# Optimization experiments

Hardware: AMD Instinct MI355X
Metric: run time of the kernel (lower is better)

Reference implementation:

```python
import jax, jax.numpy as jnp
import numpy as np

B, N, E_PER = 2048, 64, 512            # graphs, nodes/graph, edges/graph
D_NODE, D_EMB = 16, 64                 # env.node_state_dim, node_embedding_size
D_USER, D_UEMB = 32, 64                # env.user_state_dim, user_embedding_size
HID = 512
TOTAL_N, TOTAL_E = B * N, B * E_PER


def setup_inputs() -> dict:
    key = jax.random.key(0)
    ks = jax.random.split(key, 16)
    off = (jnp.arange(B, dtype=jnp.int32) * N)[:, None]
    src = jax.random.randint(ks[0], (B, E_PER), 0, N, dtype=jnp.int32) + off
    dst = jax.random.randint(ks[1], (B, E_PER), 0, N, dtype=jnp.int32) + off
    edge_index = jnp.stack([src.reshape(-1), dst.reshape(-1)])  # [2, TOTAL_E]
    s = lambda k, shape, sc=0.05: jax.random.normal(k, shape, jnp.float32) * sc
    return {
        "x": jax.random.normal(ks[2], (TOTAL_N, D_NODE), jnp.float32),
        "edge_attr": jax.random.normal(ks[3], (TOTAL_E, 2), jnp.float32),
        "user_s": jax.random.normal(ks[4], (B, D_USER), jnp.float32),
        "W_msg": s(ks[5], (D_NODE, D_EMB)), "b_msg": jnp.zeros((D_EMB,), jnp.float32),
        "W_edge": s(ks[6], (2, D_EMB)),     "b_edge": jnp.zeros((D_EMB,), jnp.float32),
        "W_self": s(ks[7], (D_NODE, D_EMB)),"b_self": jnp.zeros((D_EMB,), jnp.float32),
        "W1": s(ks[8], (D_USER, D_UEMB)),   "b1": jnp.zeros((D_UEMB,), jnp.float32),
        "W2": s(ks[9], (N * D_EMB + D_UEMB, HID)), "b2": jnp.zeros((HID,), jnp.float32),
        "W3": s(ks[10], (HID, HID // 2)),   "b3": jnp.zeros((HID // 2,), jnp.float32),
        "W4": s(ks[11], (HID // 2, N), 0.01), "b4": jnp.zeros((N,), jnp.float32),
        "edge_index": edge_index,
    }


def reference(x, edge_attr, user_s, W_msg, b_msg, W_edge, b_edge, W_self, b_self,
              W1, b1, W2, b2, W3, b3, W4, b4, edge_index):
    src, dst = edge_index[0], edge_index[1]
    # GeneralConv (PyG): msg = lin_msg(x_j) + lin_edge(e); sum-aggregate at dst; + lin_self(x_i)
    msg = x[src] @ W_msg + b_msg + edge_attr @ W_edge + b_edge          # [TOTAL_E, D_EMB]
    agg = jax.ops.segment_sum(msg, dst, num_segments=TOTAL_N)          # [TOTAL_N, D_EMB]
    node = jax.nn.relu(agg + x @ W_self + b_self)
    # F.dropout(p=0.5, training=True) -- deterministic mask for the reference
    keep = jax.random.bernoulli(jax.random.key(42), 0.5, node.shape)
    node = jnp.where(keep, node * 2.0, 0.0)
    user = jax.nn.relu(user_s @ W1 + b1)                               # [B, D_UEMB]
    states = jnp.concatenate([node.reshape(B, N * D_EMB), user], axis=1)
    h = jax.nn.relu(states @ W2 + b2)
    h = jax.nn.relu(h @ W3 + b3)
    logits = h @ W4 + b4                                               # [B, N]
    # torch: unsqueeze(dim=0) then softmax(dim=1) => softmax across the BATCH axis
    return jax.nn.softmax(logits, axis=0)[None]                        # [1, B, N]
```

## Files before the change

### kernel.cpp

```cpp
#include <hip/hip_runtime.h>
#include <stdint.h>

#define B_GRAPHS 2048
#define CHUNK 256
#define E_PER 512
#define D_USER 32
#define HID 512
#define GK 4160
#define STATES_DIM 4160
#define WS_FALLBACK 6356992
#define WS_FAST 52006912

typedef unsigned short u16;
typedef unsigned int u32;
typedef __attribute__((ext_vector_type(8))) short short8;
typedef __attribute__((ext_vector_type(4))) float f32x4;

__device__ __forceinline__ float bf2f(u16 b) {
    union { uint32_t u; float f; } c; c.u = ((uint32_t)b) << 16; return c.f;
}
__device__ __forceinline__ u16 f2bf(float f) {
    union { float f; uint32_t u; } c; c.f = f;
    uint32_t u = c.u;
    return (u16)((u + 0x7FFFu + ((u >> 16) & 1u)) >> 16);
}
__device__ __forceinline__ void unpack2(uint32_t w, float& lo, float& hi) {
    union { uint32_t u; float f; } a, b;
    a.u = w << 16; b.u = w & 0xFFFF0000u;
    lo = a.f; hi = b.f;
}

__device__ __forceinline__ uint32_t rotl32(uint32_t v, int r) {
    return (v << r) | (v >> (32 - r));
}
__device__ __forceinline__ void threefry_0_42(uint32_t x0, uint32_t x1,
                                              uint32_t& o0, uint32_t& o1) {
    const uint32_t ks0 = 0u, ks1 = 42u, ks2 = 0x1BD11BDAu ^ 42u;
    x0 += ks0; x1 += ks1;
#define TFR(r) { x0 += x1; x1 = rotl32(x1, (r)); x1 ^= x0; }
    TFR(13) TFR(15) TFR(26) TFR(6)
    x0 += ks1; x1 += ks2 + 1u;
    TFR(17) TFR(29) TFR(16) TFR(24)
    x0 += ks2; x1 += ks0 + 2u;
    TFR(13) TFR(15) TFR(26) TFR(6)
    x0 += ks0; x1 += ks1 + 3u;
    TFR(17) TFR(29) TFR(16) TFR(24)
    x0 += ks1; x1 += ks2 + 4u;
    TFR(13) TFR(15) TFR(26) TFR(6)
    x0 += ks2; x1 += ks0 + 5u;
#undef TFR
    o0 = x0; o1 = x1;
}
__device__ __forceinline__ bool keep_bit(uint32_t j) {
    uint32_t o0, o1;
    threefry_0_42(0u, j, o0, o1);
    return (((o0 ^ o1) >> 31) == 0u);
}

__global__ __launch_bounds__(256) void fill_kernel(float* __restrict__ out, float v, int n) {
    int i = blockIdx.x * 256 + threadIdx.x;
    if (i < n) out[i] = v;
}

__device__ __forceinline__ void trans32(float (*sT)[33],
                                        const float* __restrict__ W,
                                        u16* __restrict__ WT,
                                        int K, int N, int k0, int n0, int tid) {
    const int tr = tid >> 5, tc = tid & 31;
    #pragma unroll
    for (int i = 0; i < 32; i += 8)
        sT[tr + i][tc] = W[(size_t)(k0 + tr + i) * N + n0 + tc];
    __syncthreads();
    #pragma unroll
    for (int i = 0; i < 32; i += 8)
        WT[(size_t)(n0 + tr + i) * K + k0 + tc] = f2bf(sT[tc][tr + i]);
}

__global__ __launch_bounds__(256) void prep_kernel(
    const float* __restrict__ W2, u16* __restrict__ W2T,
    const float* __restrict__ W3, u16* __restrict__ W3T,
    const float* __restrict__ W4, u16* __restrict__ W4T,
    const float* __restrict__ W_msg, const float* __restrict__ W_self,
    u16* __restrict__ WcatT)
{
    __shared__ float sT[32][33];
    const int tid = threadIdx.x;
    int b = blockIdx.x;
    if (b < 2080) {
        trans32(sT, W2, W2T, 4160, 512, (b % 130) * 32, (b / 130) * 32, tid);
        return;
    }
    b -= 2080;
    if (b < 128) {
        trans32(sT, W3, W3T, 512, 256, (b % 16) * 32, (b / 16) * 32, tid);
        return;
    }
    b -= 128;
    if (b < 16) {
        trans32(sT, W4, W4T, 256, 64, (b % 8) * 32, (b / 8) * 32, tid);
        return;
    }
    #pragma unroll
    for (int i = 0; i < 8; ++i) {
        int idx = tid + 256 * i;
        int e = idx >> 5, k = idx & 31;
        float v = (k < 16) ? W_msg[k * 64 + e] : W_self[(k - 16) * 64 + e];
        WcatT[idx] = f2bf(v);
    }
}

__global__ __launch_bounds__(256) void node_fast(
    const float* __restrict__ x, const float* __restrict__ edge_attr,
    const float* __restrict__ user_s,
    const float* __restrict__ b_msg, const float* __restrict__ W_edge,
    const float* __restrict__ b_edge, const float* __restrict__ b_self,
    const float* __restrict__ W1, const float* __restrict__ b1,
    const int* __restrict__ src, const int* __restrict__ dst,
    const u16* __restrict__ WcatT,
    u16* __restrict__ states)
{
    const int g = blockIdx.x;
    const int tid = threadIdx.x;
    const int w = tid >> 6, lane = tid & 63;
    const int lm = lane & 15, q = lane >> 4;

    __shared__ u32 scnt[64][32];
    __shared__ u16 sxT[16][72];
    __shared__ u16 sA2[64][40];
    __shared__ float sesum[2][64];
    __shared__ float sdeg[64];
    __shared__ unsigned long long smask[64];

    const float* xg = x + (size_t)g * 1024;
    const float4 xv = *(const float4*)&xg[tid * 4];
    const int ge0 = g * E_PER + tid, ge1 = ge0 + 256;
    const int s0 = src[ge0] - g * 64, d0 = dst[ge0] - g * 64;
    const int s1 = src[ge1] - g * 64, d1 = dst[ge1] - g * 64;
    const float2* ea2 = (const float2*)edge_attr;
    const float2 a0 = ea2[ge0], a1 = ea2[ge1];
    float bs[4], bm[4], we0[4], we1[4];
    #pragma unroll
    for (int nt = 0; nt < 4; ++nt) {
        int e = nt * 16 + lm;
        bs[nt]  = b_self[e];
        bm[nt]  = b_msg[e] + b_edge[e];
        we0[nt] = W_edge[e];
        we1[nt] = W_edge[64 + e];
    }
    {
        uint4 z = make_uint4(0, 0, 0, 0);
        u32* c0 = &scnt[0][0] + tid * 8;
        *(uint4*)(c0) = z; *(uint4*)(c0 + 4) = z;
    }
    if (tid < 128) ((float*)sesum)[tid] = 0.f;
    {
        const int n = tid >> 2, kb = (tid & 3) * 4;
        u16 x0 = f2bf(xv.x), x1 = f2bf(xv.y), x2 = f2bf(xv.z), x3 = f2bf(xv.w);
        sxT[kb + 0][n] = x0; sxT[kb + 1][n] = x1;
        sxT[kb + 2][n] = x2; sxT[kb + 3][n] = x3;
        *(ushort4*)&sA2[n][16 + kb] = make_ushort4(x0, x1, x2, x3);
    }
    #pragma unroll 4
    for (int i = 0; i < 16; ++i) {
        unsigned long long b =
            __ballot(keep_bit((uint32_t)g * 4096u + (uint32_t)(i * 256 + tid)));
        if (lane == 0) smask[i * 4 + w] = b;
    }
    __syncthreads();

    atomicAdd(&scnt[d0][(s0 >> 1) ^ ((d0 & 7) << 2)], 1u << ((s0 & 1) * 16));
    atomicAdd(&scnt[d1][(s1 >> 1) ^ ((d1 & 7) << 2)], 1u << ((s1 & 1) * 16));
    atomicAdd(&sesum[0][d0], a0.x);
    atomicAdd(&sesum[1][d0], a0.y);
    atomicAdd(&sesum[0][d1], a1.x);
    atomicAdd(&sesum[1][d1], a1.y);
    __syncthreads();

    {
        const int d = tid >> 2, sq = tid & 3;
        uint4 c0 = *(const uint4*)&scnt[d][sq * 8];
        uint4 c1 = *(const uint4*)&scnt[d][sq * 8 + 4];
        u32 cw[8] = {c0.x, c0.y, c0.z, c0.w, c1.x, c1.y, c1.z, c1.w};
        u32 pk[8];
        float degp = 0.f;
        #pragma unroll
        for (int j = 0; j < 8; ++j) {
            u32 lo = cw[j] & 0xFFFFu, hi = cw[j] >> 16;
            degp += (float)(lo + hi);
            pk[j] = (u32)f2bf((float)lo) | ((u32)f2bf((float)hi) << 16);
        }
        *(uint4*)&scnt[d][sq * 8]     = make_uint4(pk[0], pk[1], pk[2], pk[3]);
        *(uint4*)&scnt[d][sq * 8 + 4] = make_uint4(pk[4], pk[5], pk[6], pk[7]);
        degp += __shfl_xor(degp, 1, 64);
        degp += __shfl_xor(degp, 2, 64);
        if (sq == 0) sdeg[d] = degp;
    }

    f32x4 accS;
    #pragma unroll
    for (int r = 0; r < 4; ++r) accS[r] = 0.f;
    {
        const char* crow = (const char*)&scnt[16 * w + lm][0];
        const int sw = (lm & 7) << 4;
        #pragma unroll
        for (int kh = 0; kh < 2; ++kh) {
            short8 a = *(const short8*)(crow + (((kh * 64) + q * 16) ^ sw));
            short8 b = *(const short8*)&sxT[lm][kh * 32 + q * 8];
            accS = __builtin_amdgcn_mfma_f32_16x16x32_bf16(a, b, accS, 0, 0, 0);
        }
    }
    #pragma unroll
    for (int r = 0; r < 4; ++r)
        sA2[16 * w + q * 4 + r][lm] = f2bf(accS[r]);

    f32x4 acc2[4];
    #pragma unroll
    for (int nt = 0; nt < 4; ++nt)
        #pragma unroll
        for (int r = 0; r < 4; ++r) acc2[nt][r] = 0.f;
    short8 a2 = *(const short8*)&sA2[16 * w + lm][q * 8];
    #pragma unroll
    for (int nt = 0; nt < 4; ++nt) {
        short8 b2 = *(const short8*)&WcatT[(nt * 16 + lm) * 32 + q * 8];
        acc2[nt] = __builtin_amdgcn_mfma_f32_16x16x32_bf16(a2, b2, acc2[nt], 0, 0, 0);
    }

    u16* out = states + (size_t)g * STATES_DIM;
    #pragma unroll
    for (int r = 0; r < 4; ++r) {
        int n = 16 * w + q * 4 + r;
        float dg = sdeg[n], e0 = sesum[0][n], e1 = sesum[1][n];
        unsigned long long m = smask[n];
        #pragma unroll
        for (int nt = 0; nt < 4; ++nt) {
            float v = acc2[nt][r] + bs[nt] + dg * bm[nt]
                    + e0 * we0[nt] + e1 * we1[nt];
            v = v > 0.f ? v : 0.f;
            int e = nt * 16 + lm;
            v = ((m >> e) & 1ull) ? v * 2.0f : 0.0f;
            out[n * 64 + e] = f2bf(v);
        }
    }
    if (tid < 64) {
        float v = b1[tid];
        const float* us = user_s + (size_t)g * D_USER;
        #pragma unroll
        for (int k = 0; k < D_USER; ++k) v += us[k] * W1[k * 64 + tid];
        out[4096 + tid] = f2bf(v > 0.f ? v : 0.f);
    }
}

__global__ __launch_bounds__(256) void node_fb(
    int g0,
    const float* __restrict__ x, const float* __restrict__ edge_attr,
    const float* __restrict__ user_s,
    const float* __restrict__ W_msg, const float* __restrict__ b_msg,
    const float* __restrict__ W_edge, const float* __restrict__ b_edge,
    const float* __restrict__ W_self, const float* __restrict__ b_self,
    const float* __restrict__ W1, const float* __restrict__ b1,
    const int* __restrict__ src, const int* __restrict__ dst,
    float* __restrict__ states)
{
    const int g = g0 + blockIdx.x;
    const int tid = threadIdx.x;

    __shared__ float sx[64][16];
    __shared__ float sxsum[64][16];
    __shared__ float sesum[64][2];
    __shared__ float sdeg[64];
    __shared__ float sWmsg[16][64];
    __shared__ float sWself[16][64];
    __shared__ float sWedge[2][64];
    __shared__ float sbias[64];
    __shared__ float sbself[64];

    const float* xg = x + (size_t)g * 1024;
    for (int i = tid; i < 1024; i += 256) {
        sx[i >> 4][i & 15] = xg[i];
        ((float*)sxsum)[i] = 0.f;
        ((float*)sWmsg)[i] = W_msg[i];
        ((float*)sWself)[i] = W_self[i];
    }
    if (tid < 128) ((float*)sWedge)[tid] = W_edge[tid];
    if (tid < 64) {
        sbias[tid] = b_msg[tid] + b_edge[tid];
        sbself[tid] = b_self[tid];
        sdeg[tid] = 0.f;
        sesum[tid][0] = 0.f; sesum[tid][1] = 0.f;
    }
    __syncthreads();

    const float2* ea2 = (const float2*)edge_attr;
    for (int e = tid; e < E_PER; e += 256) {
        int ge = g * E_PER + e;
        int s = src[ge] - g * 64;
        int d = dst[ge] - g * 64;
        float2 a = ea2[ge];
        atomicAdd(&sdeg[d], 1.0f);
        atomicAdd(&sesum[d][0], a.x);
        atomicAdd(&sesum[d][1], a.y);
        #pragma unroll
        for (int k = 0; k < 16; ++k) atomicAdd(&sxsum[d][k], sx[s][k]);
    }
    __syncthreads();

    float* out = states + (size_t)blockIdx.x * STATES_DIM;
    #pragma unroll
    for (int i = 0; i < 16; ++i) {
        int idx = tid + 256 * i;
        int n = idx >> 6, e = idx & 63;
        float v = sbself[e] + sdeg[n] * sbias[e]
                + sesum[n][0] * sWedge[0][e] + sesum[n][1] * sWedge[1][e];
        #pragma unroll
        for (int k = 0; k < 16; ++k)
            v += sxsum[n][k] * sWmsg[k][e] + sx[n][k] * sWself[k][e];
        v = v > 0.f ? v : 0.f;
        v = keep_bit((uint32_t)g * 4096u + (uint32_t)idx) ? v * 2.0f : 0.0f;
        out[idx] = v;
    }
    if (tid < 64) {
        float v = b1[tid];
        const float* us = user_s + (size_t)g * D_USER;
        #pragma unroll
        for (int k = 0; k < D_USER; ++k) v += us[k] * W1[k * 64 + tid];
        out[4096 + tid] = v > 0.f ? v : 0.f;
    }
}

__global__ __launch_bounds__(256) void gemm64(
    const u16* __restrict__ A, const u16* __restrict__ BT,
    float* __restrict__ Cpart, int K, int Ksplit, int N, int ntiles,
    int pstride)
{
    const int cpx = gridDim.x >> 3;
    const int bid = blockIdx.x;
    const int wg  = (bid & 7) * cpx + (bid >> 3);
    const int nt  = wg % ntiles, mt = wg / ntiles;
    const int m0 = mt * 64, n0 = nt * 64;
    const int kb = blockIdx.y * Ksplit;

    __shared__ u16 sA[64][72];
    __shared__ u16 sB[64][72];

    const int tid = threadIdx.x;
    const int wave = tid >> 6, lane = tid & 63;
    const int wm = (wave & 1) * 32, wn = (wave >> 1) * 32;
    const int lm = lane & 15, q = lane >> 4;

    f32x4 acc00, acc01, acc10, acc11;
    #pragma unroll
    for (int r = 0; r < 4; ++r) {
        acc00[r] = 0.f; acc01[r] = 0.f; acc10[r] = 0.f; acc11[r] = 0.f;
    }

    const int arow = tid >> 2, aseg = (tid & 3) * 16;
    const u16* pa = &A [(size_t)(m0 + arow) * K + kb + aseg];
    const u16* pb = &BT[(size_t)(n0 + arow) * K + kb + aseg];
    uint4 ra0 = *(const uint4*)pa, ra1 = *(const uint4*)(pa + 8);
    uint4 rb0 = *(const uint4*)pb, rb1 = *(const uint4*)(pb + 8);

    for (int k0 = 0; k0 < Ksplit; k0 += 64) {
        __syncthreads();
        *(uint4*)&sA[arow][aseg]     = ra0;
        *(uint4*)&sA[arow][aseg + 8] = ra1;
        *(uint4*)&sB[arow][aseg]     = rb0;
        *(uint4*)&sB[arow][aseg + 8] = rb1;
        __syncthreads();
        if (k0 + 64 < Ksplit) {
            pa += 64; pb += 64;
            ra0 = *(const uint4*)pa; ra1 = *(const uint4*)(pa + 8);
            rb0 = *(const uint4*)pb; rb1 = *(const uint4*)(pb + 8);
        }
        #pragma unroll
        for (int kh = 0; kh < 2; ++kh) {
            short8 a0 = *(const short8*)&sA[wm + lm]     [kh * 32 + q * 8];
            short8 a1 = *(const short8*)&sA[wm + 16 + lm][kh * 32 + q * 8];
            short8 b0 = *(const short8*)&sB[wn + lm]     [kh * 32 + q * 8];
            short8 b1 = *(const short8*)&sB[wn + 16 + lm][kh * 32 + q * 8];
            acc00 = __builtin_amdgcn_mfma_f32_16x16x32_bf16(a0, b0, acc00, 0, 0, 0);
            acc01 = __builtin_amdgcn_mfma_f32_16x16x32_bf16(a0, b1, acc01, 0, 0, 0);
            acc10 = __builtin_amdgcn_mfma_f32_16x16x32_bf16(a1, b0, acc10, 0, 0, 0);
            acc11 = __builtin_amdgcn_mfma_f32_16x16x32_bf16(a1, b1, acc11, 0, 0, 0);
        }
    }

    float* Cp = Cpart + (size_t)blockIdx.y * pstride;
    #pragma unroll
    for (int r = 0; r < 4; ++r) {
        int m = m0 + wm + q * 4 + r;
        Cp[(size_t)m * N + n0 + wn + lm]              = acc00[r];
        Cp[(size_t)m * N + n0 + wn + 16 + lm]         = acc01[r];
        Cp[(size_t)(m + 16) * N + n0 + wn + lm]       = acc10[r];
        Cp[(size_t)(m + 16) * N + n0 + wn + 16 + lm]  = acc11[r];
    }
}

__global__ __launch_bounds__(256) void bias_relu_sum(
    const float* __restrict__ parts, int pstride, int nsplit,
    const float* __restrict__ bias, u16* __restrict__ out,
    int Nmask, int total4)
{
    int i = blockIdx.x * 256 + threadIdx.x;
    if (i >= total4) return;
    const int base = i * 4;
    float4 v = *(const float4*)&bias[base & Nmask];
    for (int s = 0; s < nsplit; ++s) {
        float4 p = *(const float4*)&parts[(size_t)s * pstride + base];
        v.x += p.x; v.y += p.y; v.z += p.z; v.w += p.w;
    }
    ushort4 o;
    o.x = f2bf(v.x > 0.f ? v.x : 0.f);
    o.y = f2bf(v.y > 0.f ? v.y : 0.f);
    o.z = f2bf(v.z > 0.f ? v.z : 0.f);
    o.w = f2bf(v.w > 0.f ? v.w : 0.f);
    *(ushort4*)&out[base] = o;
}

template<typename AT, typename CT, bool RELU>
__global__ __launch_bounds__(256) void gemm_any(
    const AT* __restrict__ A, const float* __restrict__ B,
    const float* __restrict__ bias, CT* __restrict__ C,
    int M, int N, int K)
{
    __shared__ float sA[32][72];
    __shared__ float sB[32][64];

    const int tid = threadIdx.x;
    const int tx = tid & 15;
    const int ty = tid >> 4;
    const int m0 = blockIdx.x * 64, n0 = blockIdx.y * 64;

    float acc[4][4] = {};

    for (int k0 = 0; k0 < K; k0 += 32) {
        if constexpr (sizeof(AT) == 4) {
            int r = tid >> 3;
            int c = (tid & 7) * 4;
            #pragma unroll
            for (int rr = 0; rr < 64; rr += 32) {
                float4 v = *(const float4*)&((const float*)A)[(size_t)(m0 + r + rr) * K + k0 + c];
                sA[c + 0][r + rr] = v.x; sA[c + 1][r + rr] = v.y;
                sA[c + 2][r + rr] = v.z; sA[c + 3][r + rr] = v.w;
            }
        } else {
            int m = tid >> 2;
            int c = (tid & 3) * 8;
            uint4 v = *(const uint4*)&((const u16*)A)[(size_t)(m0 + m) * K + k0 + c];
            unpack2(v.x, sA[c + 0][m], sA[c + 1][m]);
            unpack2(v.y, sA[c + 2][m], sA[c + 3][m]);
            unpack2(v.z, sA[c + 4][m], sA[c + 5][m]);
            unpack2(v.w, sA[c + 6][m], sA[c + 7][m]);
        }
        {
            int r = tid >> 3;
            int nc = (tid & 7) * 8;
            float4 v0 = *(const float4*)&B[(size_t)(k0 + r) * N + n0 + nc];
            float4 v1 = *(const float4*)&B[(size_t)(k0 + r) * N + n0 + nc + 4];
            sB[r][nc + 0] = v0.x; sB[r][nc + 1] = v0.y;
            sB[r][nc + 2] = v0.z; sB[r][nc + 3] = v0.w;
            sB[r][nc + 4] = v1.x; sB[r][nc + 5] = v1.y;
            sB[r][nc + 6] = v1.z; sB[r][nc + 7] = v1.w;
        }
        __syncthreads();
        #pragma unroll
        for (int kk = 0; kk < 32; ++kk) {
            float4 av = *(const float4*)&sA[kk][ty * 4];
            float4 bv = *(const float4*)&sB[kk][tx * 4];
            float a_[4] = {av.x, av.y, av.z, av.w};
            float b_[4] = {bv.x, bv.y, bv.z, bv.w};
            #pragma unroll
            for (int i = 0; i < 4; ++i)
                #pragma unroll
                for (int j = 0; j < 4; ++j)
                    acc[i][j] += a_[i] * b_[j];
        }
        __syncthreads();
    }

    #pragma unroll
    for (int i = 0; i < 4; ++i) {
        int m = m0 + ty * 4 + i;
        #pragma unroll
        for (int j = 0; j < 4; ++j) {
            int n = n0 + tx * 4 + j;
            float v = acc[i][j] + bias[n];
            if (RELU) v = v > 0.f ? v : 0.f;
            if constexpr (sizeof(CT) == 2) C[(size_t)m * N + n] = (CT)f2bf(v);
            else                           C[(size_t)m * N + n] = (CT)v;
        }
    }
}

__global__ __launch_bounds__(256) void softmax4(
    const float* __restrict__ parts, const float* __restrict__ b4,
    float* __restrict__ out)
{
    const int n = blockIdx.x;
    const int tid = threadIdx.x;
    __shared__ float sred[4];
    const int wid = tid >> 6, lane = tid & 63;
    const float bn = b4[n];

    float v[8];
    #pragma unroll
    for (int i = 0; i < 8; ++i) {
        int row = (tid + 256 * i) * 64 + n;
        float t = bn + parts[row] + parts[131072 + row]
                + parts[262144 + row] + parts[393216 + row];
        v[i] = (t > -1e30f && t < 1e30f) ? t : 0.0f;
    }

    float mx = -3.4e38f;
    #pragma unroll
    for (int i = 0; i < 8; ++i) mx = fmaxf(mx, v[i]);
    #pragma unroll
    for (int off = 32; off > 0; off >>= 1) mx = fmaxf(mx, __shfl_down(mx, off, 64));
    if (lane == 0) sred[wid] = mx;
    __syncthreads();
    if (tid == 0) sred[0] = fmaxf(fmaxf(sred[0], sred[1]), fmaxf(sred[2], sred[3]));
    __syncthreads();
    mx = sred[0];
    __syncthreads();

    float sum = 0.f;
    #pragma unroll
    for (int i = 0; i < 8; ++i) { v[i] = expf(v[i] - mx); sum += v[i]; }
    #pragma unroll
    for (int off = 32; off > 0; off >>= 1) sum += __shfl_down(sum, off, 64);
    if (lane == 0) sred[wid] = sum;
    __syncthreads();
    if (tid == 0) sred[0] = sred[0] + sred[1] + sred[2] + sred[3];
    __syncthreads();
    float inv = 1.0f / sred[0];
    #pragma unroll
    for (int i = 0; i < 8; ++i) out[(tid + 256 * i) * 64 + n] = v[i] * inv;
}

__global__ __launch_bounds__(256) void softmax_kernel(
    const float* __restrict__ logits, float* __restrict__ out)
{
    const int n = blockIdx.x;
    const int tid = threadIdx.x;
    __shared__ float sred[4];
    const int wid = tid >> 6, lane = tid & 63;

    float v[8];
    #pragma unroll
    for (int i = 0; i < 8; ++i) {
        float t = logits[(tid + 256 * i) * 64 + n];
        v[i] = (t > -1e30f && t < 1e30f) ? t : 0.0f;
    }

    float mx = -3.4e38f;
    #pragma unroll
    for (int i = 0; i < 8; ++i) mx = fmaxf(mx, v[i]);
    #pragma unroll
    for (int off = 32; off > 0; off >>= 1) mx = fmaxf(mx, __shfl_down(mx, off, 64));
    if (lane == 0) sred[wid] = mx;
    __syncthreads();
    if (tid == 0) sred[0] = fmaxf(fmaxf(sred[0], sred[1]), fmaxf(sred[2], sred[3]));
    __syncthreads();
    mx = sred[0];
    __syncthreads();

    float sum = 0.f;
    #pragma unroll
    for (int i = 0; i < 8; ++i) { v[i] = expf(v[i] - mx); sum += v[i]; }
    #pragma unroll
    for (int off = 32; off > 0; off >>= 1) sum += __shfl_down(sum, off, 64);
    if (lane == 0) sred[wid] = sum;
    __syncthreads();
    if (tid == 0) sred[0] = sred[0] + sred[1] + sred[2] + sred[3];
    __syncthreads();
    float inv = 1.0f / sred[0];
    #pragma unroll
    for (int i = 0; i < 8; ++i) out[(tid + 256 * i) * 64 + n] = v[i] * inv;
}

extern "C" void kernel_launch(void* const* d_in, const int* in_sizes, int n_in,
                              void* d_out, int out_size, void* d_ws, size_t ws_size,
                              hipStream_t stream) {
    if (ws_size < (size_t)WS_FALLBACK || n_in < 18) {
        fill_kernel<<<(out_size + 255) / 256, 256, 0, stream>>>((float*)d_out, 0.25f, out_size);
        return;
    }
    {
        const int expect[18] = {2097152, 2097152, 65536, 1024, 64, 128, 64,
                                1024, 64, 2048, 64, 2129920, 512, 131072, 256,
                                16384, 64, 2097152};
        bool ok = true;
        for (int i = 0; i < 18; ++i) ok = ok && (in_sizes[i] == expect[i]);
        if (!ok || out_size != 131072) {
            fill_kernel<<<(out_size + 255) / 256, 256, 0, stream>>>((float*)d_out, 0.125f, out_size);
            return;
        }
    }

    const float* x         = (const float*)d_in[0];
    const float* edge_attr = (const float*)d_in[1];
    const float* user_s    = (const float*)d_in[2];
    const float* W_msg     = (const float*)d_in[3];
    const float* b_msg     = (const float*)d_in[4];
    const float* W_edge    = (const float*)d_in[5];
    const float* b_edge    = (const float*)d_in[6];
    const float* W_self    = (const float*)d_in[7];
    const float* b_self    = (const float*)d_in[8];
    const float* W1        = (const float*)d_in[9];
    const float* b1        = (const float*)d_in[10];
    const float* W2        = (const float*)d_in[11];
    const float* b2        = (const float*)d_in[12];
    const float* W3        = (const float*)d_in[13];
    const float* b3        = (const float*)d_in[14];
    const float* W4        = (const float*)d_in[15];
    const float* b4        = (const float*)d_in[16];
    const int* edge_index  = (const int*)d_in[17];
    const int* src = edge_index;
    const int* dst = edge_index + B_GRAPHS * E_PER;

    float* logits = (float*)d_out;
    char* ws = (char*)d_ws;

    if (ws_size >= (size_t)WS_FAST) {
        u16*   states = (u16*)ws;
        u16*   W2T    = (u16*)(ws + 17039360);
        float* h2part = (float*)(ws + 21299200);
        u16*   h2     = (u16*)(ws + 42270720);
        u16*   W3T    = (u16*)(ws + 44367872);
        float* h3part = (float*)(ws + 44630016);
        u16*   h3     = (u16*)(ws + 48824320);
        u16*   WcatT  = (u16*)(ws + 49872896);
        u16*   W4T    = (u16*)(ws + 49876992);
        float* lpart  = (float*)(ws + 49909760);

        prep_kernel<<<2225, 256, 0, stream>>>(W2, W2T, W3, W3T, W4, W4T,
                                              W_msg, W_self, WcatT);
        node_fast<<<B_GRAPHS, 256, 0, stream>>>(
            x, edge_attr, user_s, b_msg, W_edge, b_edge, b_self, W1, b1,
            src, dst, WcatT, states);
        gemm64<<<dim3(256, 5), 256, 0, stream>>>(states, W2T, h2part,
                                                 GK, 832, 512, 8, 1048576);
        bias_relu_sum<<<1024, 256, 0, stream>>>(h2part, 1048576, 5, b2, h2,
                                                511, 262144);
        gemm64<<<dim3(128, 2), 256, 0, stream>>>(h2, W3T, h3part,
                                                 512, 256, 256, 4, 524288);
        bias_relu_sum<<<512, 256, 0, stream>>>(h3part, 524288, 2, b3, h3,
                                               255, 131072);
        gemm64<<<dim3(32, 4), 256, 0, stream>>>(h3, W4T, lpart,
                                                256, 64, 64, 1, 131072);
        softmax4<<<64, 256, 0, stream>>>(lpart, b4, logits);
    } else {
        float* states = (float*)ws;
        float* h3     = (float*)ws;
        u16*   h2     = (u16*)(ws + 4259840);

        for (int c = 0; c < B_GRAPHS / CHUNK; ++c) {
            node_fb<<<CHUNK, 256, 0, stream>>>(
                c * CHUNK, x, edge_attr, user_s, W_msg, b_msg, W_edge, b_edge,
                W_self, b_self, W1, b1, src, dst, states);
            gemm_any<float, u16, true><<<dim3(CHUNK / 64, HID / 64), 256, 0, stream>>>(
                states, W2, b2, h2 + (size_t)c * CHUNK * HID, CHUNK, HID, STATES_DIM);
        }
        gemm_any<u16,   float, true ><<<dim3(32, 4), 256, 0, stream>>>(
            h2, W3, b3, h3, B_GRAPHS, HID / 2, HID);
        gemm_any<float, float, false><<<dim3(32, 1), 256, 0, stream>>>(
            h3, W4, b4, logits, B_GRAPHS, 64, HID / 2);
        softmax_kernel<<<64, 256, 0, stream>>>(logits, logits);
    }
}
```

Measured before the change: 186.4 us.

## Fuse weight-transpose prep into node kernel and rebalance W3 split-K

Merges the separate weight transpose/convert kernel into the node embedding kernel as extra blocks, removing one launch and the dependency between them. Each node block now builds its own Wcat tile in shared memory instead of reading it from a global buffer, and the dropout keep bits are computed inline instead of through a ballot-filled shared mask. The W3 GEMM's split-K factor goes from 2 to 4, with a matching partial-sum reduction, to give it more parallelism. In exchange it adds redundant per-block Wcat construction, more hash work per output element, and a larger workspace for the extra partials.

```diff
diff --git a/kernel.cpp b/kernel.cpp
--- a/kernel.cpp
+++ b/kernel.cpp
@@ -9,7 +9,7 @@
 #define GK 4160
 #define STATES_DIM 4160
 #define WS_FALLBACK 6356992
-#define WS_FAST 52006912
+#define WS_FAST 56197120
 
 typedef unsigned short u16;
 typedef unsigned int u32;
@@ -76,60 +76,57 @@
         WT[(size_t)(n0 + tr + i) * K + k0 + tc] = f2bf(sT[tc][tr + i]);
 }
 
-__global__ __launch_bounds__(256) void prep_kernel(
-    const float* __restrict__ W2, u16* __restrict__ W2T,
-    const float* __restrict__ W3, u16* __restrict__ W3T,
-    const float* __restrict__ W4, u16* __restrict__ W4T,
-    const float* __restrict__ W_msg, const float* __restrict__ W_self,
-    u16* __restrict__ WcatT)
-{
-    __shared__ float sT[32][33];
-    const int tid = threadIdx.x;
-    int b = blockIdx.x;
-    if (b < 2080) {
-        trans32(sT, W2, W2T, 4160, 512, (b % 130) * 32, (b / 130) * 32, tid);
-        return;
-    }
-    b -= 2080;
-    if (b < 128) {
-        trans32(sT, W3, W3T, 512, 256, (b % 16) * 32, (b / 16) * 32, tid);
-        return;
-    }
-    b -= 128;
-    if (b < 16) {
-        trans32(sT, W4, W4T, 256, 64, (b % 8) * 32, (b / 8) * 32, tid);
-        return;
-    }
-    #pragma unroll
-    for (int i = 0; i < 8; ++i) {
-        int idx = tid + 256 * i;
-        int e = idx >> 5, k = idx & 31;
-        float v = (k < 16) ? W_msg[k * 64 + e] : W_self[(k - 16) * 64 + e];
-        WcatT[idx] = f2bf(v);
-    }
-}
-
-__global__ __launch_bounds__(256) void node_fast(
+#define SM_SCNT  0
+#define SM_SXT   8192
+#define SM_SA2   10496
+#define SM_WCAT  15616
+#define SM_ESUM  20736
+#define SM_DEG   21248
+#define SM_SIZE  21504
+
+__global__ __launch_bounds__(256) void node_prep(
     const float* __restrict__ x, const float* __restrict__ edge_attr,
     const float* __restrict__ user_s,
+    const float* __restrict__ W_msg, const float* __restrict__ W_self,
     const float* __restrict__ b_msg, const float* __restrict__ W_edge,
     const float* __restrict__ b_edge, const float* __restrict__ b_self,
     const float* __restrict__ W1, const float* __restrict__ b1,
     const int* __restrict__ src, const int* __restrict__ dst,
-    const u16* __restrict__ WcatT,
+    const float* __restrict__ W2, u16* __restrict__ W2T,
+    const float* __restrict__ W3, u16* __restrict__ W3T,
+    const float* __restrict__ W4, u16* __restrict__ W4T,
     u16* __restrict__ states)
 {
+    __shared__ __align__(16) char smem[SM_SIZE];
+    const int tid = threadIdx.x;
+
+    if (blockIdx.x >= B_GRAPHS) {
+        float (*sT)[33] = (float(*)[33])smem;
+        int b = blockIdx.x - B_GRAPHS;
+        if (b < 2080) {
+            trans32(sT, W2, W2T, 4160, 512, (b % 130) * 32, (b / 130) * 32, tid);
+            return;
+        }
+        b -= 2080;
+        if (b < 128) {
+            trans32(sT, W3, W3T, 512, 256, (b % 16) * 32, (b / 16) * 32, tid);
+            return;
+        }
+        b -= 128;
+        trans32(sT, W4, W4T, 256, 64, (b % 8) * 32, (b / 8) * 32, tid);
+        return;
+    }
+
+    u32 (*scnt)[32]  = (u32(*)[32])(smem + SM_SCNT);
+    u16 (*sxT)[72]   = (u16(*)[72])(smem + SM_SXT);
+    u16 (*sA2)[40]   = (u16(*)[40])(smem + SM_SA2);
+    u16* sWcat       = (u16*)(smem + SM_WCAT);
+    float (*sesum)[64] = (float(*)[64])(smem + SM_ESUM);
+    float* sdeg      = (float*)(smem + SM_DEG);
+
     const int g = blockIdx.x;
-    const int tid = threadIdx.x;
     const int w = tid >> 6, lane = tid & 63;
     const int lm = lane & 15, q = lane >> 4;
-
-    __shared__ u32 scnt[64][32];
-    __shared__ u16 sxT[16][72];
-    __shared__ u16 sA2[64][40];
-    __shared__ float sesum[2][64];
-    __shared__ float sdeg[64];
-    __shared__ unsigned long long smask[64];
 
     const float* xg = x + (size_t)g * 1024;
     const float4 xv = *(const float4*)&xg[tid * 4];
@@ -154,17 +151,20 @@
     }
     if (tid < 128) ((float*)sesum)[tid] = 0.f;
     {
+        #pragma unroll
+        for (int i = 0; i < 8; ++i) {
+            int idx = tid + 256 * i;
+            int e = idx >> 5, k = idx & 31;
+            float v = (k < 16) ? W_msg[k * 64 + e] : W_self[(k - 16) * 64 + e];
+            sWcat[e * 40 + k] = f2bf(v);
+        }
+    }
+    {
         const int n = tid >> 2, kb = (tid & 3) * 4;
         u16 x0 = f2bf(xv.x), x1 = f2bf(xv.y), x2 = f2bf(xv.z), x3 = f2bf(xv.w);
         sxT[kb + 0][n] = x0; sxT[kb + 1][n] = x1;
         sxT[kb + 2][n] = x2; sxT[kb + 3][n] = x3;
         *(ushort4*)&sA2[n][16 + kb] = make_ushort4(x0, x1, x2, x3);
-    }
-    #pragma unroll 4
-    for (int i = 0; i < 16; ++i) {
-        unsigned long long b =
-            __ballot(keep_bit((uint32_t)g * 4096u + (uint32_t)(i * 256 + tid)));
-        if (lane == 0) smask[i * 4 + w] = b;
     }
     __syncthreads();
 
@@ -221,7 +221,7 @@
     short8 a2 = *(const short8*)&sA2[16 * w + lm][q * 8];
     #pragma unroll
     for (int nt = 0; nt < 4; ++nt) {
-        short8 b2 = *(const short8*)&WcatT[(nt * 16 + lm) * 32 + q * 8];
+        short8 b2 = *(const short8*)&sWcat[(nt * 16 + lm) * 40 + q * 8];
         acc2[nt] = __builtin_amdgcn_mfma_f32_16x16x32_bf16(a2, b2, acc2[nt], 0, 0, 0);
     }
 
@@ -230,15 +230,14 @@
     for (int r = 0; r < 4; ++r) {
         int n = 16 * w + q * 4 + r;
         float dg = sdeg[n], e0 = sesum[0][n], e1 = sesum[1][n];
-        unsigned long long m = smask[n];
+        uint32_t jbase = (uint32_t)g * 4096u + (uint32_t)(n * 64 + lm);
         #pragma unroll
         for (int nt = 0; nt < 4; ++nt) {
             float v = acc2[nt][r] + bs[nt] + dg * bm[nt]
                     + e0 * we0[nt] + e1 * we1[nt];
             v = v > 0.f ? v : 0.f;
-            int e = nt * 16 + lm;
-            v = ((m >> e) & 1ull) ? v * 2.0f : 0.0f;
-            out[n * 64 + e] = f2bf(v);
+            v = keep_bit(jbase + (uint32_t)(nt * 16)) ? v * 2.0f : 0.0f;
+            out[n * 64 + nt * 16 + lm] = f2bf(v);
         }
     }
     if (tid < 64) {
@@ -627,23 +626,20 @@
         u16*   h2     = (u16*)(ws + 42270720);
         u16*   W3T    = (u16*)(ws + 44367872);
         float* h3part = (float*)(ws + 44630016);
-        u16*   h3     = (u16*)(ws + 48824320);
-        u16*   WcatT  = (u16*)(ws + 49872896);
-        u16*   W4T    = (u16*)(ws + 49876992);
-        float* lpart  = (float*)(ws + 49909760);
-
-        prep_kernel<<<2225, 256, 0, stream>>>(W2, W2T, W3, W3T, W4, W4T,
-                                              W_msg, W_self, WcatT);
-        node_fast<<<B_GRAPHS, 256, 0, stream>>>(
-            x, edge_attr, user_s, b_msg, W_edge, b_edge, b_self, W1, b1,
-            src, dst, WcatT, states);
+        u16*   h3     = (u16*)(ws + 53018624);
+        u16*   W4T    = (u16*)(ws + 54067200);
+        float* lpart  = (float*)(ws + 54099968);
+
+        node_prep<<<B_GRAPHS + 2224, 256, 0, stream>>>(
+            x, edge_attr, user_s, W_msg, W_self, b_msg, W_edge, b_edge,
+            b_self, W1, b1, src, dst, W2, W2T, W3, W3T, W4, W4T, states);
         gemm64<<<dim3(256, 5), 256, 0, stream>>>(states, W2T, h2part,
                                                  GK, 832, 512, 8, 1048576);
         bias_relu_sum<<<1024, 256, 0, stream>>>(h2part, 1048576, 5, b2, h2,
                                                 511, 262144);
-        gemm64<<<dim3(128, 2), 256, 0, stream>>>(h2, W3T, h3part,
-                                                 512, 256, 256, 4, 524288);
-        bias_relu_sum<<<512, 256, 0, stream>>>(h3part, 524288, 2, b3, h3,
+        gemm64<<<dim3(128, 4), 256, 0, stream>>>(h2, W3T, h3part,
+                                                 512, 128, 256, 4, 524288);
+        bias_relu_sum<<<512, 256, 0, stream>>>(h3part, 524288, 4, b3, h3,
                                                255, 131072);
         gemm64<<<dim3(32, 4), 256, 0, stream>>>(h3, W4T, lpart,
                                                 256, 64, 64, 1, 131072);
```

Result: faster. 174.7 us (median of 2 runs) (-6.2%).
